# Optimization experiments

Hardware: AMD Instinct MI355X
Metric: run time of the kernel (lower is better)

Reference implementation:

```python
import jax, jax.numpy as jnp
import numpy as np

DIM = 128
WIN = (2, 7, 7)
HEADS = 4
N = WIN[0] * WIN[1] * WIN[2]  # 98
B_ = 2048
NW = 256  # num windows per sample; B_ // NW = batch = 8


def _relative_position_index(win):
    t = np.arange(win[0]); h = np.arange(win[1]); w = np.arange(win[2])
    coords = np.stack(np.meshgrid(t, h, w, indexing='ij'))  # (3, T, H, W)
    cf = coords.reshape(3, -1)  # (3, N)
    rel = cf[:, :, None] - cf[:, None, :]  # (3, N, N)
    rel = rel.transpose(1, 2, 0).copy()
    rel[:, :, 0] += win[0] - 1
    rel[:, :, 1] += win[1] - 1
    rel[:, :, 2] += win[2] - 1
    rel[:, :, 0] *= (2 * win[1] - 1) * (2 * win[2] - 1)
    rel[:, :, 1] *= 2 * win[2] - 1
    return rel.sum(-1).astype(np.int32)  # (N, N)


def setup_inputs() -> dict:
    key = jax.random.key(0)
    ks = jax.random.split(key, 8)
    table_len = (2 * WIN[0] - 1) * (2 * WIN[1] - 1) * (2 * WIN[2] - 1)  # 507
    x = jax.random.normal(ks[0], (B_, N, DIM), dtype=jnp.float32)
    # 0 / -inf style additive mask (use -1e4 as finite -inf)
    u = jax.random.uniform(ks[1], (NW, N, N))
    mask = jnp.where(u < 0.9, 0.0, -1e4).astype(jnp.float32)
    qkv_w = jax.random.normal(ks[2], (3 * DIM, DIM), dtype=jnp.float32) * (DIM ** -0.5)
    qkv_b = jax.random.normal(ks[3], (3 * DIM,), dtype=jnp.float32) * 0.02
    proj_w = jax.random.normal(ks[4], (DIM, DIM), dtype=jnp.float32) * (DIM ** -0.5)
    proj_b = jax.random.normal(ks[5], (DIM,), dtype=jnp.float32) * 0.02
    bias_table = jax.random.normal(ks[6], (table_len, HEADS), dtype=jnp.float32) * 0.02
    rel_index = jnp.asarray(_relative_position_index(WIN))
    return {"x": x, "mask": mask, "qkv_w": qkv_w, "qkv_b": qkv_b,
            "proj_w": proj_w, "proj_b": proj_b, "bias_table": bias_table,
            "rel_index": rel_index}


def reference(x, mask, qkv_w, qkv_b, proj_w, proj_b, bias_table, rel_index):
    Bq, n, c = x.shape
    hd = c // HEADS
    scale = hd ** -0.5
    qkv = x @ qkv_w.T + qkv_b  # (B_, N, 3C)
    qkv = qkv.reshape(Bq, n, 3, HEADS, hd).transpose(2, 0, 3, 1, 4)  # (3, B_, H, N, hd)
    q, k, v = qkv[0] * scale, qkv[1], qkv[2]
    attn = jnp.einsum('bhnd,bhmd->bhnm', q, k)  # (B_, H, N, N)
    bias = bias_table[rel_index.reshape(-1)].reshape(n, n, HEADS)
    attn = attn + bias.transpose(2, 0, 1)[None]  # add (1, H, N, N)
    nW = mask.shape[0]
    attn = attn.reshape(Bq // nW, nW, HEADS, n, n) + mask[None, :, None]
    attn = jax.nn.softmax(attn.reshape(Bq, HEADS, n, n), axis=-1)
    out = jnp.einsum('bhnm,bhmd->bhnd', attn, v)  # (B_, H, N, hd)
    out = out.transpose(0, 2, 1, 3).reshape(Bq, n, c)
    return out @ proj_w.T + proj_b
```

## Files before the change

kernel.cpp:

```cpp
#include <hip/hip_runtime.h>
#include <hip/hip_bf16.h>


#define NTOK 98
#define NN (NTOK * NTOK)
#define SCALE 0.17677669529663687f
#define LOG2E 1.4426950408889634f

typedef short bf16x8 __attribute__((ext_vector_type(8)));
typedef float f32x4 __attribute__((ext_vector_type(4)));
#define MFMA(a, b, c) __builtin_amdgcn_mfma_f32_16x16x32_bf16(a, b, c, 0, 0, 0)

static __device__ __forceinline__ unsigned short f2bf(float f) {
  union { float f; unsigned int i; } x; x.f = f;
  unsigned int u = x.i;
  unsigned int rnd = ((u >> 16) & 1u) + 0x7fffu;
  return (unsigned short)((u + rnd) >> 16);
}

static __device__ __forceinline__ unsigned int cvt_pk_bf16(float lo, float hi) {
  unsigned int pk;
  asm("v_cvt_pk_bf16_f32 %0, %1, %2" : "=v"(pk) : "v"(lo), "v"(hi));
  return pk;
}

__global__ void k0_w(const float* __restrict__ qkv_w, const float* __restrict__ proj_w,
                     unsigned short* __restrict__ wqb, unsigned short* __restrict__ wpb) {
  int idx = blockIdx.x * 256 + threadIdx.x;
  if (idx < 49152) {
    wqb[idx] = f2bf(qkv_w[idx]);
  } else {
    int m2 = idx - 49152;
    int m = m2 & 127;
    int pim = (m & ~31) | ((m & 1) << 4) | ((m & 31) >> 1);
    wpb[m2] = f2bf(proj_w[(m2 & ~127) | pim]);
  }
}

__global__ void k0b_bm(const float* __restrict__ table, const int* __restrict__ rel,
                       const float* __restrict__ mask, unsigned int* __restrict__ bm) {
  const int wmodh = blockIdx.x, mt = blockIdx.y;
  const int wmod = wmodh >> 2, h = wmodh & 3;
  unsigned int* dst = bm + (size_t)(wmodh * 7 + mt) * 896;
  for (int u = threadIdx.x; u < 896; u += 256) {
    int w = u & 1, lane = (u >> 1) & 63, nt = u >> 7;
    int quad = lane >> 4, L15 = lane & 15;
    int col = nt * 16 + L15;
    unsigned int pk = 0;
#pragma unroll
    for (int rr = 0; rr < 2; ++rr) {
      int row = mt * 16 + quad * 4 + 2 * w + rr;
      float v = -1.0e30f;
      if (row < NTOK && col < NTOK) {
        int nm = row * NTOK + col;
        v = (table[rel[nm] * 4 + h] + mask[(size_t)wmod * NN + nm]) * LOG2E;
      }
      pk |= ((unsigned int)f2bf(v)) << (16 * rr);
    }
    dst[u] = pk;
  }
}

__global__ __launch_bounds__(256) void k1_qkv(const float* __restrict__ x,
                                              const unsigned short* __restrict__ wqb,
                                              const float* __restrict__ qkv_b,
                                              unsigned short* __restrict__ q,
                                              unsigned short* __restrict__ k,
                                              unsigned short* __restrict__ v) {
  __shared__ unsigned short xt[64 * 136];
  __shared__ unsigned short wt[128 * 136];
  const int t = threadIdx.x;
  const int r0 = blockIdx.x * 64;
  const int wv = t >> 6, lane = t & 63, L15 = lane & 15, quad = lane >> 4;

#pragma unroll
  for (int i = 0; i < 8; ++i) {
    int idx = t + (i << 8);
    int row = idx >> 5, c4 = idx & 31;
    float4 xv = *(const float4*)&x[(size_t)(r0 + row) * 128 + c4 * 4];
    uint2 pk; pk.x = cvt_pk_bf16(xv.x, xv.y); pk.y = cvt_pk_bf16(xv.z, xv.w);
    *(uint2*)&xt[row * 136 + c4 * 4] = pk;
  }

  bf16x8 af[4];
  bool afLoaded = false;

  for (int g = 0; g < 3; ++g) {
    if (g) __syncthreads();
#pragma unroll
    for (int i = 0; i < 8; ++i) {
      int idx = t + (i << 8);
      int c = idx >> 4, kq = idx & 15;
      *(uint4*)&wt[c * 136 + kq * 8] = ((const uint4*)wqb)[g * 2048 + idx];
    }
    __syncthreads();
    if (!afLoaded) {
      afLoaded = true;
#pragma unroll
      for (int kt = 0; kt < 4; ++kt)
        af[kt] = *(const bf16x8*)&xt[(wv * 16 + L15) * 136 + kt * 32 + quad * 8];
    }

    f32x4 acc[8];
#pragma unroll
    for (int nt = 0; nt < 8; ++nt) {
      f32x4 a = {0.f, 0.f, 0.f, 0.f};
#pragma unroll
      for (int kt = 0; kt < 4; ++kt) {
        bf16x8 bf_ = *(const bf16x8*)&wt[(nt * 16 + L15) * 136 + kt * 32 + quad * 8];
        a = MFMA(af[kt], bf_, a);
      }
      acc[nt] = a;
    }

    unsigned int* dst32 = (unsigned int*)((g == 0) ? q : ((g == 1) ? k : v));
    const float sc = (g == 0) ? (SCALE * LOG2E) : 1.0f;
    float bsc[8];
#pragma unroll
    for (int nt = 0; nt < 8; ++nt) bsc[nt] = qkv_b[g * 128 + nt * 16 + L15] * sc;
#pragma unroll
    for (int reg = 0; reg < 4; ++reg) {
      int R = r0 + wv * 16 + quad * 4 + reg;
      int b = R / NTOK, n = R - b * NTOK;
      size_t base32 = ((size_t)b * 4 * NTOK + n) * 16;
#pragma unroll
      for (int h2 = 0; h2 < 4; ++h2) {
        float v0 = acc[2 * h2][reg] * sc + bsc[2 * h2];
        float v1 = acc[2 * h2 + 1][reg] * sc + bsc[2 * h2 + 1];
        dst32[base32 + (size_t)h2 * (NTOK * 16) + L15] = cvt_pk_bf16(v0, v1);
      }
    }
  }
}

__global__ __launch_bounds__(256, 4) void k2_attn(const unsigned short* __restrict__ qg,
                                                  const unsigned short* __restrict__ kg,
                                                  const unsigned short* __restrict__ vg,
                                                  const unsigned int* __restrict__ bm16,
                                                  unsigned short* __restrict__ og) {
  __shared__ unsigned short sK[112 * 40];
  __shared__ unsigned short sVt[32 * 136];
  __shared__ unsigned short sP[4 * 16 * 136];
  const int t = threadIdx.x;
  const int wmodh = blockIdx.x;
  const int wmod = wmodh >> 2, h = wmodh & 3;
  const int wv = t >> 6, lane = t & 63, L15 = lane & 15, quad = lane >> 4;
  unsigned short* myP = sP + wv * (16 * 136);

  for (int i = t; i < 280; i += 256) ((unsigned int*)sK)[1960 + i] = 0;
  for (int j = lane; j < 128; j += 64) {
    int r = j >> 3, cp = j & 7;
    *(unsigned int*)&myP[r * 136 + 112 + cp * 2] = 0;
  }
  for (int i = t; i < 32 * 30; i += 256) {
    int d = i / 30, nl = 98 + i % 30;
    int swz = ((d >> 3) & 3) << 3;
    sVt[d * 136 + (nl ^ swz)] = 0;
  }

  const int s0 = wv * 2, s1 = wv * 2 + 1;
  uint2 bmA[7], bmB[7];
  {
    const uint2* p0 = (const uint2*)(bm16 + (size_t)(wmodh * 7 + s0) * 896);
#pragma unroll
    for (int nt = 0; nt < 7; ++nt) bmA[nt] = p0[nt * 64 + lane];
    if (wv < 3) {
      const uint2* p1 = (const uint2*)(bm16 + (size_t)(wmodh * 7 + s1) * 896);
#pragma unroll
      for (int nt = 0; nt < 7; ++nt) bmB[nt] = p1[nt * 64 + lane];
    }
  }

  const int i0 = t, i1 = t + 256;
  uint4 rk0, rk1, rv0, rv1;
  auto loadKV = [&](int bh) {
    const uint4* kp = (const uint4*)kg + (size_t)bh * 392;
    const uint4* vp = (const uint4*)vg + (size_t)bh * 392;
    rk0 = kp[i0]; rv0 = vp[i0];
    if (i1 < 392) { rk1 = kp[i1]; rv1 = vp[i1]; }
  };
  bf16x8 qA0, qB0, qA1, qB1;
  auto loadQ = [&](int bh, bf16x8& qa, bf16x8& qb) {
    const size_t base = (size_t)bh * (NTOK * 32);
    qa = *(const bf16x8*)&qg[base + (size_t)(s0 * 16 + L15) * 32 + quad * 8];
    if (wv < 3) qb = *(const bf16x8*)&qg[base + (size_t)(s1 * 16 + L15) * 32 + quad * 8];
  };
  loadKV(wmod * 4 + h);
  loadQ(wmod * 4 + h, qA0, qB0);

  auto strip = [&](int mt, const uint2* bmp, bf16x8 aq, int bw) {
    f32x4 s[7];
    __builtin_amdgcn_s_setprio(1);
#pragma unroll
    for (int nt = 0; nt < 7; ++nt) {
      uint2 pkb = bmp[nt];
      f32x4 c;
      c[0] = __uint_as_float(pkb.x << 16);
      c[1] = __uint_as_float(pkb.x & 0xffff0000u);
      c[2] = __uint_as_float(pkb.y << 16);
      c[3] = __uint_as_float(pkb.y & 0xffff0000u);
      bf16x8 bk = *(const bf16x8*)&sK[(nt * 16 + L15) * 40 + quad * 8];
      s[nt] = MFMA(aq, bk, c);
    }
    __builtin_amdgcn_s_setprio(0);
    float rsv[4];
#pragma unroll
    for (int reg = 0; reg < 4; ++reg) {
      float sum = 0.f;
#pragma unroll
      for (int nt = 0; nt < 7; ++nt) {
        float e = __builtin_amdgcn_exp2f(s[nt][reg]);
        s[nt][reg] = e; sum += e;
      }
#pragma unroll
      for (int d = 1; d < 16; d <<= 1) sum += __shfl_xor(sum, d, 64);
      rsv[reg] = __builtin_amdgcn_rcpf(sum);
      unsigned short* pr = myP + (quad * 4 + reg) * 136 + L15;
#pragma unroll
      for (int p = 0; p < 4; ++p) {
        int n1 = (p < 3) ? 2 * p + 1 : 2 * p;
        unsigned int pk = cvt_pk_bf16(s[2 * p][reg], s[n1][reg]);
        pr[2 * p * 16] = (unsigned short)pk;
        if (p < 3) pr[n1 * 16] = (unsigned short)(pk >> 16);
      }
    }
    const int sw0 = (L15 >> 3) << 3;
    const int sw1 = (((16 + L15) >> 3) & 3) << 3;
    f32x4 o0 = {0.f, 0.f, 0.f, 0.f}, o1 = {0.f, 0.f, 0.f, 0.f};
    __builtin_amdgcn_s_setprio(1);
#pragma unroll
    for (int kt = 0; kt < 4; ++kt) {
      int cb = kt * 32 + quad * 8;
      bf16x8 ap  = *(const bf16x8*)&myP[L15 * 136 + cb];
      bf16x8 bv0 = *(const bf16x8*)&sVt[L15 * 136 + (cb ^ sw0)];
      bf16x8 bv1 = *(const bf16x8*)&sVt[(16 + L15) * 136 + (cb ^ sw1)];
      o0 = MFMA(ap, bv0, o0);
      o1 = MFMA(ap, bv1, o1);
    }
    __builtin_amdgcn_s_setprio(0);
#pragma unroll
    for (int reg = 0; reg < 4; ++reg) {
      int n = mt * 16 + quad * 4 + reg;
      if (n < NTOK) {
        float a0 = o0[reg] * rsv[reg], a1 = o1[reg] * rsv[reg];
        ((unsigned int*)og)[(size_t)(bw * NTOK + n) * 64 + h * 16 + L15] =
            cvt_pk_bf16(a0, a1);
      }
    }
  };

  for (int it = 0; it < 8; ++it) {
    const int bw = wmod + (it << 8);

    if (it) __syncthreads();
    {
      int row = i0 >> 2, kq = i0 & 3;
      *(uint4*)&sK[row * 40 + kq * 8] = rk0;
      int n = i0 >> 2, j0 = (i0 & 3) << 2;
      const unsigned int* pw = (const unsigned int*)&rv0;
#pragma unroll
      for (int j = 0; j < 4; ++j) {
        int dlo = j0 + j, dhi = dlo + 16;
        sVt[dlo * 136 + (n ^ (((dlo >> 3) & 3) << 3))] = (unsigned short)pw[j];
        sVt[dhi * 136 + (n ^ (((dhi >> 3) & 3) << 3))] = (unsigned short)(pw[j] >> 16);
      }
      if (i1 < 392) {
        int row1 = i1 >> 2, kq1 = i1 & 3;
        *(uint4*)&sK[row1 * 40 + kq1 * 8] = rk1;
        int n_ = i1 >> 2, j0_ = (i1 & 3) << 2;
        const unsigned int* pw1 = (const unsigned int*)&rv1;
#pragma unroll
        for (int j = 0; j < 4; ++j) {
          int dlo = j0_ + j, dhi = dlo + 16;
          sVt[dlo * 136 + (n_ ^ (((dlo >> 3) & 3) << 3))] = (unsigned short)pw1[j];
          sVt[dhi * 136 + (n_ ^ (((dhi >> 3) & 3) << 3))] = (unsigned short)(pw1[j] >> 16);
        }
      }
    }
    __syncthreads();
    if (it < 7) {
      int bhn = (bw + 256) * 4 + h;
      loadKV(bhn);
      loadQ(bhn, qA1, qB1);
    }

    strip(s0, bmA, qA0, bw);
    if (wv < 3) strip(s1, bmB, qB0, bw);
    qA0 = qA1; qB0 = qB1;
  }
}

__global__ __launch_bounds__(256) void k3_proj(const unsigned short* __restrict__ og,
                                               const unsigned short* __restrict__ wpb,
                                               const float* __restrict__ pb,
                                               float* __restrict__ out) {
  __shared__ unsigned short ot[64 * 136];
  __shared__ unsigned short wt[128 * 136];
  const int t = threadIdx.x;
  const int r0 = blockIdx.x * 64;
  const int wv = t >> 6, lane = t & 63, L15 = lane & 15, quad = lane >> 4;

#pragma unroll
  for (int i = 0; i < 4; ++i) {
    int idx = t + (i << 8);
    int row = idx >> 4, kq = idx & 15;
    *(uint4*)&ot[row * 136 + kq * 8] = ((const uint4*)og)[(size_t)(r0 + row) * 16 + kq];
  }
#pragma unroll
  for (int i = 0; i < 8; ++i) {
    int idx = t + (i << 8);
    int c = idx >> 4, kq = idx & 15;
    *(uint4*)&wt[c * 136 + kq * 8] = ((const uint4*)wpb)[idx];
  }
  __syncthreads();

  bf16x8 af[4];
#pragma unroll
  for (int kt = 0; kt < 4; ++kt)
    af[kt] = *(const bf16x8*)&ot[(wv * 16 + L15) * 136 + kt * 32 + quad * 8];

  f32x4 acc[8];
#pragma unroll
  for (int nt = 0; nt < 8; ++nt) {
    f32x4 a = {0.f, 0.f, 0.f, 0.f};
#pragma unroll
    for (int kt = 0; kt < 4; ++kt) {
      bf16x8 bf_ = *(const bf16x8*)&wt[(nt * 16 + L15) * 136 + kt * 32 + quad * 8];
      a = MFMA(af[kt], bf_, a);
    }
    acc[nt] = a;
  }

  float bias[8];
#pragma unroll
  for (int nt = 0; nt < 8; ++nt) bias[nt] = pb[nt * 16 + L15];
#pragma unroll
  for (int reg = 0; reg < 4; ++reg) {
    size_t R = (size_t)(r0 + wv * 16 + quad * 4 + reg);
#pragma unroll
    for (int nt = 0; nt < 8; ++nt)
      out[R * 128 + nt * 16 + L15] = acc[nt][reg] + bias[nt];
  }
}

extern "C" void kernel_launch(void* const* d_in, const int* in_sizes, int n_in,
                              void* d_out, int out_size, void* d_ws, size_t ws_size,
                              hipStream_t stream) {
  (void)in_sizes; (void)n_in; (void)out_size; (void)ws_size;
  const float* x      = (const float*)d_in[0];
  const float* mask   = (const float*)d_in[1];
  const float* qkv_w  = (const float*)d_in[2];
  const float* qkv_b  = (const float*)d_in[3];
  const float* proj_w = (const float*)d_in[4];
  const float* proj_b = (const float*)d_in[5];
  const float* table  = (const float*)d_in[6];
  const int*   rel    = (const int*)d_in[7];
  float* out = (float*)d_out;

  const size_t QS = (size_t)2048 * 4 * NTOK * 32;
  unsigned short* q   = (unsigned short*)d_ws;
  unsigned short* k   = q + QS;
  unsigned short* v   = k + QS;
  unsigned short* o   = v + QS;
  unsigned short* wqb = o + QS;
  unsigned short* wpb = wqb + 49152;
  unsigned int* bm = (unsigned int*)d_out;

  k0_w<<<256, 256, 0, stream>>>(qkv_w, proj_w, wqb, wpb);
  k0b_bm<<<dim3(1024, 7), 256, 0, stream>>>(table, rel, mask, bm);
  k1_qkv<<<200704 / 64, 256, 0, stream>>>(x, wqb, qkv_b, q, k, v);
  k2_attn<<<1024, 256, 0, stream>>>(q, k, v, bm, o);
  k3_proj<<<200704 / 64, 256, 0, stream>>>(o, wpb, proj_b, out);
}
```

Baseline: 379.9 us.

## Load A-operands straight to registers and prefetch weights in QKV and projection GEMMs

In the QKV kernel each lane now reads its x row fragment from global memory into registers and converts it to bf16 there, with no LDS staging. The next weight group is prefetched into registers while the current group's MFMAs run. The projection kernel does the same for its O fragments, and each block now handles two 64-row tiles so the weight staging is paid once per two tiles, halving the grid. Launch bounds of 4 are added to both kernels, which adds register pressure and an extra barrier pair per group in exchange for less LDS traffic and more overlap.

```diff
diff --git a/kernel.cpp b/kernel.cpp
--- a/kernel.cpp
+++ b/kernel.cpp
@@ -61,45 +61,57 @@
   }
 }
 
-__global__ __launch_bounds__(256) void k1_qkv(const float* __restrict__ x,
-                                              const unsigned short* __restrict__ wqb,
-                                              const float* __restrict__ qkv_b,
-                                              unsigned short* __restrict__ q,
-                                              unsigned short* __restrict__ k,
-                                              unsigned short* __restrict__ v) {
-  __shared__ unsigned short xt[64 * 136];
+__global__ __launch_bounds__(256, 4) void k1_qkv(const float* __restrict__ x,
+                                                 const unsigned short* __restrict__ wqb,
+                                                 const float* __restrict__ qkv_b,
+                                                 unsigned short* __restrict__ q,
+                                                 unsigned short* __restrict__ k,
+                                                 unsigned short* __restrict__ v) {
   __shared__ unsigned short wt[128 * 136];
   const int t = threadIdx.x;
   const int r0 = blockIdx.x * 64;
   const int wv = t >> 6, lane = t & 63, L15 = lane & 15, quad = lane >> 4;
 
-#pragma unroll
-  for (int i = 0; i < 8; ++i) {
-    int idx = t + (i << 8);
-    int row = idx >> 5, c4 = idx & 31;
-    float4 xv = *(const float4*)&x[(size_t)(r0 + row) * 128 + c4 * 4];
-    uint2 pk; pk.x = cvt_pk_bf16(xv.x, xv.y); pk.y = cvt_pk_bf16(xv.z, xv.w);
-    *(uint2*)&xt[row * 136 + c4 * 4] = pk;
-  }
-
-  bf16x8 af[4];
-  bool afLoaded = false;
-
-  for (int g = 0; g < 3; ++g) {
-    if (g) __syncthreads();
+  const char* xrow = (const char*)(x + (size_t)(r0 + wv * 16 + L15) * 128);
+  uint4 xr[8];
+#pragma unroll
+  for (int kt = 0; kt < 4; ++kt) {
+    xr[2 * kt]     = *(const uint4*)(xrow + kt * 128 + quad * 32);
+    xr[2 * kt + 1] = *(const uint4*)(xrow + kt * 128 + quad * 32 + 16);
+  }
+
+  uint4 wr[8];
+  auto loadW = [&](int g) {
+#pragma unroll
+    for (int i = 0; i < 8; ++i) wr[i] = ((const uint4*)wqb)[g * 2048 + t + (i << 8)];
+  };
+  auto stageW = [&]() {
 #pragma unroll
     for (int i = 0; i < 8; ++i) {
       int idx = t + (i << 8);
       int c = idx >> 4, kq = idx & 15;
-      *(uint4*)&wt[c * 136 + kq * 8] = ((const uint4*)wqb)[g * 2048 + idx];
-    }
-    __syncthreads();
-    if (!afLoaded) {
-      afLoaded = true;
-#pragma unroll
-      for (int kt = 0; kt < 4; ++kt)
-        af[kt] = *(const bf16x8*)&xt[(wv * 16 + L15) * 136 + kt * 32 + quad * 8];
-    }
+      *(uint4*)&wt[c * 136 + kq * 8] = wr[i];
+    }
+  };
+  loadW(0);
+  stageW();
+
+  bf16x8 af[4];
+#pragma unroll
+  for (int kt = 0; kt < 4; ++kt) {
+    const float* f0 = (const float*)&xr[2 * kt];
+    const float* f1 = (const float*)&xr[2 * kt + 1];
+    union { unsigned int u[4]; bf16x8 v8; } U;
+    U.u[0] = cvt_pk_bf16(f0[0], f0[1]);
+    U.u[1] = cvt_pk_bf16(f0[2], f0[3]);
+    U.u[2] = cvt_pk_bf16(f1[0], f1[1]);
+    U.u[3] = cvt_pk_bf16(f1[2], f1[3]);
+    af[kt] = U.v8;
+  }
+  __syncthreads();
+
+  for (int g = 0; g < 3; ++g) {
+    if (g < 2) loadW(g + 1);
 
     f32x4 acc[8];
 #pragma unroll
@@ -129,6 +141,11 @@
         float v1 = acc[2 * h2 + 1][reg] * sc + bsc[2 * h2 + 1];
         dst32[base32 + (size_t)h2 * (NTOK * 16) + L15] = cvt_pk_bf16(v0, v1);
       }
+    }
+    if (g < 2) {
+      __syncthreads();
+      stageW();
+      __syncthreads();
     }
   }
 }
@@ -290,56 +307,69 @@
   }
 }
 
-__global__ __launch_bounds__(256) void k3_proj(const unsigned short* __restrict__ og,
-                                               const unsigned short* __restrict__ wpb,
-                                               const float* __restrict__ pb,
-                                               float* __restrict__ out) {
-  __shared__ unsigned short ot[64 * 136];
+__global__ __launch_bounds__(256, 4) void k3_proj(const unsigned short* __restrict__ og,
+                                                  const unsigned short* __restrict__ wpb,
+                                                  const float* __restrict__ pb,
+                                                  float* __restrict__ out) {
   __shared__ unsigned short wt[128 * 136];
   const int t = threadIdx.x;
-  const int r0 = blockIdx.x * 64;
   const int wv = t >> 6, lane = t & 63, L15 = lane & 15, quad = lane >> 4;
 
-#pragma unroll
-  for (int i = 0; i < 4; ++i) {
-    int idx = t + (i << 8);
-    int row = idx >> 4, kq = idx & 15;
-    *(uint4*)&ot[row * 136 + kq * 8] = ((const uint4*)og)[(size_t)(r0 + row) * 16 + kq];
-  }
-#pragma unroll
-  for (int i = 0; i < 8; ++i) {
-    int idx = t + (i << 8);
-    int c = idx >> 4, kq = idx & 15;
-    *(uint4*)&wt[c * 136 + kq * 8] = ((const uint4*)wpb)[idx];
-  }
+  auto loadO = [&](int r0, uint4* orr) {
+    const char* orow = (const char*)og + (size_t)(r0 + wv * 16 + L15) * 256;
+#pragma unroll
+    for (int kt = 0; kt < 4; ++kt)
+      orr[kt] = *(const uint4*)(orow + kt * 64 + quad * 16);
+  };
+
+  const int r0a = blockIdx.x * 64;
+  const int r0b = r0a + 1568 * 64;
+  uint4 orA[4], orB[4];
+  loadO(r0a, orA);
+  {
+    uint4 wr[8];
+#pragma unroll
+    for (int i = 0; i < 8; ++i) wr[i] = ((const uint4*)wpb)[t + (i << 8)];
+#pragma unroll
+    for (int i = 0; i < 8; ++i) {
+      int idx = t + (i << 8);
+      int c = idx >> 4, kq = idx & 15;
+      *(uint4*)&wt[c * 136 + kq * 8] = wr[i];
+    }
+  }
+  loadO(r0b, orB);
+
+  float bias[8];
+#pragma unroll
+  for (int nt = 0; nt < 8; ++nt) bias[nt] = pb[nt * 16 + L15];
   __syncthreads();
 
-  bf16x8 af[4];
-#pragma unroll
-  for (int kt = 0; kt < 4; ++kt)
-    af[kt] = *(const bf16x8*)&ot[(wv * 16 + L15) * 136 + kt * 32 + quad * 8];
-
-  f32x4 acc[8];
-#pragma unroll
-  for (int nt = 0; nt < 8; ++nt) {
-    f32x4 a = {0.f, 0.f, 0.f, 0.f};
-#pragma unroll
-    for (int kt = 0; kt < 4; ++kt) {
-      bf16x8 bf_ = *(const bf16x8*)&wt[(nt * 16 + L15) * 136 + kt * 32 + quad * 8];
-      a = MFMA(af[kt], bf_, a);
-    }
-    acc[nt] = a;
-  }
-
-  float bias[8];
-#pragma unroll
-  for (int nt = 0; nt < 8; ++nt) bias[nt] = pb[nt * 16 + L15];
-#pragma unroll
-  for (int reg = 0; reg < 4; ++reg) {
-    size_t R = (size_t)(r0 + wv * 16 + quad * 4 + reg);
-#pragma unroll
-    for (int nt = 0; nt < 8; ++nt)
-      out[R * 128 + nt * 16 + L15] = acc[nt][reg] + bias[nt];
+#pragma unroll
+  for (int half = 0; half < 2; ++half) {
+    const uint4* orr = half ? orB : orA;
+    const int r0 = half ? r0b : r0a;
+    bf16x8 af[4];
+#pragma unroll
+    for (int kt = 0; kt < 4; ++kt) af[kt] = *(const bf16x8*)&orr[kt];
+
+    f32x4 acc[8];
+#pragma unroll
+    for (int nt = 0; nt < 8; ++nt) {
+      f32x4 a = {0.f, 0.f, 0.f, 0.f};
+#pragma unroll
+      for (int kt = 0; kt < 4; ++kt) {
+        bf16x8 bf_ = *(const bf16x8*)&wt[(nt * 16 + L15) * 136 + kt * 32 + quad * 8];
+        a = MFMA(af[kt], bf_, a);
+      }
+      acc[nt] = a;
+    }
+#pragma unroll
+    for (int reg = 0; reg < 4; ++reg) {
+      size_t R = (size_t)(r0 + wv * 16 + quad * 4 + reg);
+#pragma unroll
+      for (int nt = 0; nt < 8; ++nt)
+        out[R * 128 + nt * 16 + L15] = acc[nt][reg] + bias[nt];
+    }
   }
 }
 
@@ -370,5 +400,5 @@
   k0b_bm<<<dim3(1024, 7), 256, 0, stream>>>(table, rel, mask, bm);
   k1_qkv<<<200704 / 64, 256, 0, stream>>>(x, wqb, qkv_b, q, k, v);
   k2_attn<<<1024, 256, 0, stream>>>(q, k, v, bm, o);
-  k3_proj<<<200704 / 64, 256, 0, stream>>>(o, wpb, proj_b, out);
-}
+  k3_proj<<<1568, 256, 0, stream>>>(o, wpb, proj_b, out);
+}
```

Result: slower. 467.3 us (+23.0%).
